# Kernel optimization log

Hardware: AMD Instinct MI355X
Metric: run time of the kernel (lower is better)

The kernel has to match this reference:

```python
import math
import jax, jax.numpy as jnp
import numpy as np

L, H, C, D, FF = 12, 12, 768, 64, 3072   # layers, heads, d_model, head_dim, 4*d_model
B, T = 2, 2048
CHUNK = 16
VP = CHUNK ** 3 + 2   # pos vocab (+BOS/EOS) = 4098
VF = 4096             # feature codebook


def setup_inputs() -> dict:
    key = jax.random.key(0)
    ks = jax.random.split(key, 16)
    s = 0.02
    return {
        "tokens": jax.random.randint(ks[0], (B, T), 0, VF, dtype=jnp.int32),
        "coords": jax.random.randint(ks[1], (B, T, 3), 0, CHUNK, dtype=jnp.int32),
        "token_type": jax.random.randint(ks[2], (B, T), 0, 2, dtype=jnp.int32),
        "pos_emb_w": jax.random.normal(ks[3], (VP, C), jnp.float32),
        "feat_emb_w": jax.random.normal(ks[4], (VF, C), jnp.float32),
        "qkv_w": jax.random.normal(ks[5], (L, 3 * C, C), jnp.float32) * s,
        "out_w": jax.random.normal(ks[6], (L, C, C), jnp.float32) * s,
        "q_scale": jnp.ones((L, D), jnp.float32),
        "k_scale": jnp.ones((L, D), jnp.float32),
        "ln1_w": jnp.ones((L, C), jnp.float32), "ln1_b": jnp.zeros((L, C), jnp.float32),
        "ln2_w": jnp.ones((L, C), jnp.float32), "ln2_b": jnp.zeros((L, C), jnp.float32),
        "fc1_w": jax.random.normal(ks[7], (L, FF, C), jnp.float32) * s,
        "fc2_w": jax.random.normal(ks[8], (L, C, FF), jnp.float32) * s,
        "res_a": jnp.ones((L,), jnp.float32), "res_m": jnp.ones((L,), jnp.float32),
        "skip_a": jnp.full((L,), 0.1, jnp.float32), "skip_m": jnp.full((L,), 0.1, jnp.float32),
        "lnf_w": jnp.ones((C,), jnp.float32), "lnf_b": jnp.zeros((C,), jnp.float32),
        "pos_head_w": jax.random.normal(ks[9], (VP, C), jnp.float32) * 0.001,
        "feat_head_w": jax.random.normal(ks[10], (VF, C), jnp.float32) * 0.001,
    }


def _ln(x, w, b):
    m = x.mean(-1, keepdims=True)
    v = ((x - m) ** 2).mean(-1, keepdims=True)
    return (x - m) / jnp.sqrt(v + 1e-5) * w + b


def _qknorm(x, scale):
    # per-head RMSNorm in fp32, eps added before sqrt (matches torch QKNorm)
    x32 = x.astype(jnp.float32)
    n = jnp.sqrt((x32 * x32).mean(-1, keepdims=True) + 1e-6)
    return x32 / n * scale


def _rope3d(x, coords):
    # x: (B,H,T,D); coords: (B,T,3) int voxel coords.
    # Split head_dim into 3 axis groups of `half` rotation pairs; tail dims pass through.
    half = D // 6            # pairs per axis (10 for D=64)
    rot = 3 * half           # total rotated pairs (30) -> 60 rotated dims, 4 untouched
    inv_freq = 1.0 / (10000.0 ** (jnp.arange(half, dtype=jnp.float32) / half))
    ang = coords.astype(jnp.float32)[..., :, None] * inv_freq      # (B,T,3,half)
    ang = ang.reshape(coords.shape[0], coords.shape[1], rot)        # (B,T,rot)
    cos = jnp.cos(ang)[:, None]                                     # (B,1,T,rot)
    sin = jnp.sin(ang)[:, None]
    xr = x[..., : 2 * rot].reshape(*x.shape[:-1], rot, 2)
    x1, x2 = xr[..., 0], xr[..., 1]
    rot_out = jnp.stack([x1 * cos - x2 * sin, x1 * sin + x2 * cos], axis=-1)
    rot_out = rot_out.reshape(*x.shape[:-1], 2 * rot)
    return jnp.concatenate([rot_out, x[..., 2 * rot:]], axis=-1)


def _forward(tokens, coords, token_type, pos_emb_w, feat_emb_w, qkv_w, out_w, q_scale,
             k_scale, ln1_w, ln1_b, ln2_w, ln2_b, fc1_w, fc2_w, res_a, res_m,
             skip_a, skip_m, lnf_w, lnf_b, pos_head_w, feat_head_w):
    is_feat = (token_type == 1)[..., None]
    x = jnp.where(is_feat,
                  feat_emb_w[jnp.clip(tokens, 0, VF - 1)],
                  pos_emb_w[jnp.clip(tokens, 0, VP - 1)])        # (B,T,C)
    mask = jnp.tril(jnp.ones((T, T), bool))
    scale = 1.0 / math.sqrt(D)

    def blk(x, p):
        qw, ow, qs, kcs, l1w, l1b, l2w, l2b, f1, f2, ra, rm, sa, sm = p
        h = _ln(x, l1w, l1b)
        qkv = h @ qw.T                                           # (B,T,3C)
        q, k, v = jnp.split(qkv, 3, axis=-1)
        to_heads = lambda t: t.reshape(B, T, H, D).transpose(0, 2, 1, 3)
        q, k, v = to_heads(q), to_heads(k), to_heads(v)
        q = _rope3d(_qknorm(q, qs), coords)
        k = _rope3d(_qknorm(k, kcs), coords)
        att = jnp.einsum('bhqd,bhkd->bhqk', q, k) * scale
        att = jax.nn.softmax(jnp.where(mask, att, -1e30), axis=-1)
        o = jnp.einsum('bhqk,bhkd->bhqd', att, v)
        o = o.transpose(0, 2, 1, 3).reshape(B, T, C) @ ow.T
        x = sa * x + ra * o
        h2 = _ln(x, l2w, l2b)
        m = jax.nn.gelu(h2 @ f1.T, approximate=False) @ f2.T
        x = sm * x + rm * m
        return x, None

    x, _ = jax.lax.scan(blk, x, (qkv_w, out_w, q_scale, k_scale, ln1_w, ln1_b,
                                 ln2_w, ln2_b, fc1_w, fc2_w, res_a, res_m,
                                 skip_a, skip_m))
    x = _ln(x, lnf_w, lnf_b)
    return x @ pos_head_w.T, x @ feat_head_w.T


def reference(tokens, coords, token_type, pos_emb_w, feat_emb_w, qkv_w, out_w,
              q_scale, k_scale, ln1_w, ln1_b, ln2_w, ln2_b, fc1_w, fc2_w,
              res_a, res_m, skip_a, skip_m, lnf_w, lnf_b, pos_head_w, feat_head_w):
    return _forward(tokens, coords, token_type, pos_emb_w, feat_emb_w, qkv_w, out_w,
                    q_scale, k_scale, ln1_w, ln1_b, ln2_w, ln2_b, fc1_w, fc2_w,
                    res_a, res_m, skip_a, skip_m, lnf_w, lnf_b, pos_head_w, feat_head_w)
```

## Files before the change

### kernel.cpp

```cpp
#include <hip/hip_runtime.h>
#include <math.h>

constexpr int B_  = 2;
constexpr int T_  = 2048;
constexpr int H_  = 12;
constexpr int C_  = 768;
constexpr int D_  = 64;
constexpr int FF_ = 3072;
constexpr int L_  = 12;
constexpr int VP_ = 4098;
constexpr int VF_ = 4096;
constexpr int BT_ = B_ * T_;

__global__ __launch_bounds__(256) void embed_kernel(
    const int* __restrict__ tokens, const int* __restrict__ ttype,
    const float* __restrict__ pos_w, const float* __restrict__ feat_w,
    float* __restrict__ x) {
  int row = blockIdx.x;
  int tok = tokens[row];
  const float* src;
  if (ttype[row] == 1) {
    int t = min(max(tok, 0), VF_ - 1);
    src = feat_w + (size_t)t * C_;
  } else {
    int t = min(max(tok, 0), VP_ - 1);
    src = pos_w + (size_t)t * C_;
  }
  float* dst = x + (size_t)row * C_;
  for (int c = threadIdx.x; c < C_; c += 256) dst[c] = src[c];
}

__global__ __launch_bounds__(256) void ln_kernel(
    const float* __restrict__ x, const float* __restrict__ w,
    const float* __restrict__ b, float* __restrict__ out) {
  int row = blockIdx.x;
  const float* xr = x + (size_t)row * C_;
  float vv[3];
  float s = 0.f, s2 = 0.f;
#pragma unroll
  for (int i = 0; i < 3; i++) {
    float t = xr[threadIdx.x + i * 256];
    vv[i] = t; s += t; s2 += t * t;
  }
#pragma unroll
  for (int off = 32; off; off >>= 1) {
    s  += __shfl_xor(s,  off, 64);
    s2 += __shfl_xor(s2, off, 64);
  }
  __shared__ float ss[4], ss2[4];
  int wave = threadIdx.x >> 6, lane = threadIdx.x & 63;
  if (lane == 0) { ss[wave] = s; ss2[wave] = s2; }
  __syncthreads();
  s  = ss[0] + ss[1] + ss[2] + ss[3];
  s2 = ss2[0] + ss2[1] + ss2[2] + ss2[3];
  float mean = s * (1.f / C_);
  float var  = s2 * (1.f / C_) - mean * mean;
  float inv  = 1.f / sqrtf(var + 1e-5f);
  float* orow = out + (size_t)row * C_;
#pragma unroll
  for (int i = 0; i < 3; i++) {
    int c = threadIdx.x + i * 256;
    orow[c] = (vv[i] - mean) * inv * w[c] + b[c];
  }
}

template <int BN, int EPI>
__global__ __launch_bounds__(256) void gemm_xwT(
    const float* __restrict__ A, const float* __restrict__ W,
    float* Co, const float* resid,
    const float* __restrict__ skip_p, const float* __restrict__ rs_p,
    int M, int N, int K) {
  constexpr int BK = 16;
  constexpr int MB = 2;
  constexpr int NB = BN / 64;
  __shared__ float As[BK][132];
  __shared__ float Ws[BK][BN + 4];

  int bm = blockIdx.y * 128, bn = blockIdx.x * BN;
  int tid = threadIdx.x;
  int tn = tid & 15, tm = tid >> 4;
  int lr = tid >> 2;
  int lk = (tid & 3) * 4;

  float acc[MB][NB][4][4] = {};
  float4 ar[MB], wr[NB];

#pragma unroll
  for (int u = 0; u < MB; u++)
    ar[u] = *(const float4*)(A + (size_t)(bm + lr + 64 * u) * K + lk);
#pragma unroll
  for (int v = 0; v < NB; v++) {
    int wrow = bn + lr + 64 * v;
    wr[v] = (wrow < N) ? *(const float4*)(W + (size_t)wrow * K + lk)
                       : make_float4(0.f, 0.f, 0.f, 0.f);
  }
#pragma unroll
  for (int u = 0; u < MB; u++) {
    As[lk + 0][lr + 64 * u] = ar[u].x; As[lk + 1][lr + 64 * u] = ar[u].y;
    As[lk + 2][lr + 64 * u] = ar[u].z; As[lk + 3][lr + 64 * u] = ar[u].w;
  }
#pragma unroll
  for (int v = 0; v < NB; v++) {
    Ws[lk + 0][lr + 64 * v] = wr[v].x; Ws[lk + 1][lr + 64 * v] = wr[v].y;
    Ws[lk + 2][lr + 64 * v] = wr[v].z; Ws[lk + 3][lr + 64 * v] = wr[v].w;
  }
  __syncthreads();

  for (int k0 = 0; k0 < K; k0 += BK) {
    bool has_next = (k0 + BK < K);
    if (has_next) {
      int kn = k0 + BK;
#pragma unroll
      for (int u = 0; u < MB; u++)
        ar[u] = *(const float4*)(A + (size_t)(bm + lr + 64 * u) * K + kn + lk);
#pragma unroll
      for (int v = 0; v < NB; v++) {
        int wrow = bn + lr + 64 * v;
        wr[v] = (wrow < N) ? *(const float4*)(W + (size_t)wrow * K + kn + lk)
                           : make_float4(0.f, 0.f, 0.f, 0.f);
      }
    }
#pragma unroll
    for (int kk = 0; kk < BK; kk++) {
      float a[MB][4], b[NB][4];
#pragma unroll
      for (int u = 0; u < MB; u++) {
        float4 a4 = *(const float4*)&As[kk][u * 64 + tm * 4];
        a[u][0] = a4.x; a[u][1] = a4.y; a[u][2] = a4.z; a[u][3] = a4.w;
      }
#pragma unroll
      for (int v = 0; v < NB; v++) {
        float4 b4 = *(const float4*)&Ws[kk][v * 64 + tn * 4];
        b[v][0] = b4.x; b[v][1] = b4.y; b[v][2] = b4.z; b[v][3] = b4.w;
      }
#pragma unroll
      for (int u = 0; u < MB; u++)
#pragma unroll
        for (int v = 0; v < NB; v++)
#pragma unroll
          for (int i = 0; i < 4; i++)
#pragma unroll
            for (int j = 0; j < 4; j++)
              acc[u][v][i][j] += a[u][i] * b[v][j];
    }
    if (has_next) {
      __syncthreads();
#pragma unroll
      for (int u = 0; u < MB; u++) {
        As[lk + 0][lr + 64 * u] = ar[u].x; As[lk + 1][lr + 64 * u] = ar[u].y;
        As[lk + 2][lr + 64 * u] = ar[u].z; As[lk + 3][lr + 64 * u] = ar[u].w;
      }
#pragma unroll
      for (int v = 0; v < NB; v++) {
        Ws[lk + 0][lr + 64 * v] = wr[v].x; Ws[lk + 1][lr + 64 * v] = wr[v].y;
        Ws[lk + 2][lr + 64 * v] = wr[v].z; Ws[lk + 3][lr + 64 * v] = wr[v].w;
      }
      __syncthreads();
    }
  }

  float skip = 0.f, rs = 0.f;
  if constexpr (EPI == 2) { skip = *skip_p; rs = *rs_p; }
  bool full = (bn + BN <= N) && ((N & 3) == 0);
#pragma unroll
  for (int u = 0; u < MB; u++)
#pragma unroll
    for (int i = 0; i < 4; i++) {
      int m = bm + u * 64 + tm * 4 + i;
#pragma unroll
      for (int v = 0; v < NB; v++) {
        int n = bn + v * 64 + tn * 4;
        float c4[4];
#pragma unroll
        for (int j = 0; j < 4; j++) {
          float c = acc[u][v][i][j];
          if constexpr (EPI == 1)
            c = 0.5f * c * (1.f + erff(c * 0.70710678118654752f));
          if constexpr (EPI == 2) {
            if (n + j < N) c = skip * resid[(size_t)m * N + n + j] + rs * c;
          }
          c4[j] = c;
        }
        if (full) {
          *(float4*)(Co + (size_t)m * N + n) =
              make_float4(c4[0], c4[1], c4[2], c4[3]);
        } else {
#pragma unroll
          for (int j = 0; j < 4; j++)
            if (n + j < N) Co[(size_t)m * N + n + j] = c4[j];
        }
      }
    }
}

__global__ __launch_bounds__(256) void qknorm_rope_kernel(
    float* __restrict__ qkv, const int* __restrict__ coords,
    const float* __restrict__ qscale, const float* __restrict__ kscale) {
  int row = blockIdx.x;
  int wave = threadIdx.x >> 6, lane = threadIdx.x & 63;
  int c0 = coords[row * 3 + 0];
  int c1 = coords[row * 3 + 1];
  int c2 = coords[row * 3 + 2];
  for (int g = wave; g < 2 * H_; g += 4) {
    int h = g >> 1, isk = g & 1;
    size_t idx = (size_t)row * (3 * C_) + (size_t)isk * C_ + h * D_ + lane;
    float v = qkv[idx];
    float ssum = v * v;
#pragma unroll
    for (int off = 32; off; off >>= 1) ssum += __shfl_xor(ssum, off, 64);
    float n = sqrtf(ssum * (1.f / D_) + 1e-6f);
    const float* sc = isk ? kscale : qscale;
    float xn = v / n * sc[lane];
    float partner = __shfl_xor(xn, 1, 64);
    float outv = xn;
    if (lane < 60) {
      int p = lane >> 1;
      int axis = p / 10;
      int f = p - axis * 10;
      int crd = (axis == 0) ? c0 : ((axis == 1) ? c1 : c2);
      float invf = expf(-(float)f * 0.1f * 9.210340371976184f);
      float ang = (float)crd * invf;
      float sn, cs;
      sincosf(ang, &sn, &cs);
      if (lane & 1) {
        outv = partner * sn + xn * cs;
      } else {
        outv = xn * cs - partner * sn;
      }
    }
    qkv[idx] = outv;
  }
}

__global__ __launch_bounds__(256) void attn_kernel(
    const float* __restrict__ qkv, float* __restrict__ out) {
  int bh = blockIdx.y;
  int b = bh / H_, h = bh % H_;
  int q0 = blockIdx.x * 64;
  int tid = threadIdx.x;
  int tn = tid & 15, tm = tid >> 4;

  __shared__ float Qs[64][72];
  __shared__ float Ks[64][72];
  __shared__ float Vs[64][72];
  __shared__ float Ps[64][72];

  {
    int lr = tid >> 2;
    int ld = (tid & 3) * 16;
    const float* src = qkv + (size_t)(b * T_ + q0 + lr) * (3 * C_) + h * D_ + ld;
    const float sc = 0.125f;
#pragma unroll
    for (int u = 0; u < 4; u++) {
      float4 v = ((const float4*)src)[u];
      Qs[ld + u * 4 + 0][lr] = v.x * sc;
      Qs[ld + u * 4 + 1][lr] = v.y * sc;
      Qs[ld + u * 4 + 2][lr] = v.z * sc;
      Qs[ld + u * 4 + 3][lr] = v.w * sc;
    }
  }

  float accO[4][4] = {};
  float mrow[4], lrow[4];
#pragma unroll
  for (int i = 0; i < 4; i++) { mrow[i] = -1e30f; lrow[i] = 0.f; }

  for (int k0 = 0; k0 <= q0; k0 += 64) {
    __syncthreads();
    {
      int lr = tid >> 2;
      int ld = (tid & 3) * 16;
      const float* kb = qkv + (size_t)(b * T_ + k0 + lr) * (3 * C_) + C_ + h * D_ + ld;
#pragma unroll
      for (int u = 0; u < 4; u++) {
        float4 v = ((const float4*)kb)[u];
        Ks[ld + u * 4 + 0][lr] = v.x;
        Ks[ld + u * 4 + 1][lr] = v.y;
        Ks[ld + u * 4 + 2][lr] = v.z;
        Ks[ld + u * 4 + 3][lr] = v.w;
      }
      const float* vb = kb + C_;
#pragma unroll
      for (int u = 0; u < 4; u++) {
        *(float4*)&Vs[lr][ld + u * 4] = ((const float4*)vb)[u];
      }
    }
    __syncthreads();

    float s[4][4] = {};
#pragma unroll
    for (int d = 0; d < 64; d++) {
      float4 a4 = *(const float4*)&Qs[d][tm * 4];
      float4 b4 = *(const float4*)&Ks[d][tn * 4];
      float a[4] = {a4.x, a4.y, a4.z, a4.w};
      float bb[4] = {b4.x, b4.y, b4.z, b4.w};
#pragma unroll
      for (int i = 0; i < 4; i++)
#pragma unroll
        for (int j = 0; j < 4; j++) s[i][j] += a[i] * bb[j];
    }

    if (k0 == q0) {
#pragma unroll
      for (int i = 0; i < 4; i++)
#pragma unroll
        for (int j = 0; j < 4; j++)
          if (tn * 4 + j > tm * 4 + i) s[i][j] = -1e30f;
    }

#pragma unroll
    for (int i = 0; i < 4; i++) {
      float rm = fmaxf(fmaxf(s[i][0], s[i][1]), fmaxf(s[i][2], s[i][3]));
#pragma unroll
      for (int off = 1; off < 16; off <<= 1) rm = fmaxf(rm, __shfl_xor(rm, off, 64));
      float mnew = fmaxf(mrow[i], rm);
      float alpha = __expf(mrow[i] - mnew);
      mrow[i] = mnew;
      float rs = 0.f;
#pragma unroll
      for (int j = 0; j < 4; j++) {
        float p = __expf(s[i][j] - mnew);
        s[i][j] = p;
        rs += p;
      }
#pragma unroll
      for (int off = 1; off < 16; off <<= 1) rs += __shfl_xor(rs, off, 64);
      lrow[i] = lrow[i] * alpha + rs;
#pragma unroll
      for (int j = 0; j < 4; j++) accO[i][j] *= alpha;
    }

#pragma unroll
    for (int i = 0; i < 4; i++)
      *(float4*)&Ps[tm * 4 + i][tn * 4] = make_float4(s[i][0], s[i][1], s[i][2], s[i][3]);
    __syncthreads();

#pragma unroll
    for (int kk = 0; kk < 64; kk += 4) {
      float pi[4][4], vu[4][4];
#pragma unroll
      for (int i = 0; i < 4; i++) {
        float4 p4 = *(const float4*)&Ps[tm * 4 + i][kk];
        pi[i][0] = p4.x; pi[i][1] = p4.y; pi[i][2] = p4.z; pi[i][3] = p4.w;
      }
#pragma unroll
      for (int u = 0; u < 4; u++) {
        float4 v4 = *(const float4*)&Vs[kk + u][tn * 4];
        vu[u][0] = v4.x; vu[u][1] = v4.y; vu[u][2] = v4.z; vu[u][3] = v4.w;
      }
#pragma unroll
      for (int u = 0; u < 4; u++)
#pragma unroll
        for (int i = 0; i < 4; i++)
#pragma unroll
          for (int j = 0; j < 4; j++) accO[i][j] += pi[i][u] * vu[u][j];
    }
  }

#pragma unroll
  for (int i = 0; i < 4; i++) {
    float inv = 1.f / lrow[i];
    float4 o = make_float4(accO[i][0] * inv, accO[i][1] * inv,
                           accO[i][2] * inv, accO[i][3] * inv);
    *(float4*)(out + (size_t)(b * T_ + q0 + tm * 4 + i) * C_ + h * D_ + tn * 4) = o;
  }
}

extern "C" void kernel_launch(void* const* d_in, const int* in_sizes, int n_in,
                              void* d_out, int out_size, void* d_ws, size_t ws_size,
                              hipStream_t stream) {
  const int*   tokens    = (const int*)d_in[0];
  const int*   coords    = (const int*)d_in[1];
  const int*   ttype     = (const int*)d_in[2];
  const float* pos_emb   = (const float*)d_in[3];
  const float* feat_emb  = (const float*)d_in[4];
  const float* qkv_w     = (const float*)d_in[5];
  const float* out_w     = (const float*)d_in[6];
  const float* q_scale   = (const float*)d_in[7];
  const float* k_scale   = (const float*)d_in[8];
  const float* ln1_w     = (const float*)d_in[9];
  const float* ln1_b     = (const float*)d_in[10];
  const float* ln2_w     = (const float*)d_in[11];
  const float* ln2_b     = (const float*)d_in[12];
  const float* fc1_w     = (const float*)d_in[13];
  const float* fc2_w     = (const float*)d_in[14];
  const float* res_a     = (const float*)d_in[15];
  const float* res_m     = (const float*)d_in[16];
  const float* skip_a    = (const float*)d_in[17];
  const float* skip_m    = (const float*)d_in[18];
  const float* lnf_w     = (const float*)d_in[19];
  const float* lnf_b     = (const float*)d_in[20];
  const float* pos_head  = (const float*)d_in[21];
  const float* feat_head = (const float*)d_in[22];
  float* out = (float*)d_out;

  float* ws    = (float*)d_ws;
  float* x     = ws;
  float* hbuf  = x     + (size_t)BT_ * C_;
  float* qkvb  = hbuf  + (size_t)BT_ * C_;
  float* attnb = qkvb  + (size_t)BT_ * 3 * C_;
  float* ffb   = attnb + (size_t)BT_ * C_;

  embed_kernel<<<BT_, 256, 0, stream>>>(tokens, ttype, pos_emb, feat_emb, x);

  for (int l = 0; l < L_; l++) {
    ln_kernel<<<BT_, 256, 0, stream>>>(x, ln1_w + l * C_, ln1_b + l * C_, hbuf);
    gemm_xwT<128, 0><<<dim3((3 * C_) / 128, BT_ / 128), 256, 0, stream>>>(
        hbuf, qkv_w + (size_t)l * 3 * C_ * C_, qkvb, nullptr, nullptr, nullptr,
        BT_, 3 * C_, C_);
    qknorm_rope_kernel<<<BT_, 256, 0, stream>>>(qkvb, coords,
                                                q_scale + l * D_, k_scale + l * D_);
    attn_kernel<<<dim3(T_ / 64, B_ * H_), 256, 0, stream>>>(qkvb, attnb);
    gemm_xwT<64, 2><<<dim3(C_ / 64, BT_ / 128), 256, 0, stream>>>(
        attnb, out_w + (size_t)l * C_ * C_, x, x, skip_a + l, res_a + l,
        BT_, C_, C_);
    ln_kernel<<<BT_, 256, 0, stream>>>(x, ln2_w + l * C_, ln2_b + l * C_, hbuf);
    gemm_xwT<128, 1><<<dim3(FF_ / 128, BT_ / 128), 256, 0, stream>>>(
        hbuf, fc1_w + (size_t)l * FF_ * C_, ffb, nullptr, nullptr, nullptr,
        BT_, FF_, C_);
    gemm_xwT<64, 2><<<dim3(C_ / 64, BT_ / 128), 256, 0, stream>>>(
        ffb, fc2_w + (size_t)l * C_ * FF_, x, x, skip_m + l, res_m + l,
        BT_, C_, FF_);
  }

  ln_kernel<<<BT_, 256, 0, stream>>>(x, lnf_w, lnf_b, hbuf);
  gemm_xwT<128, 0><<<dim3((VP_ + 127) / 128, BT_ / 128), 256, 0, stream>>>(
      hbuf, pos_head, out, nullptr, nullptr, nullptr, BT_, VP_, C_);
  gemm_xwT<128, 0><<<dim3(VF_ / 128, BT_ / 128), 256, 0, stream>>>(
      hbuf, feat_head, out + (size_t)BT_ * VP_, nullptr, nullptr, nullptr,
      BT_, VF_, C_);
}
```

Before: 16.04 ms.

## Register-prefetch next K/V tile in attention and swizzle shared-memory layouts

```diff
diff --git a/kernel.cpp b/kernel.cpp
--- a/kernel.cpp
+++ b/kernel.cpp
@@ -232,6 +232,8 @@
   }
 }
 
+constexpr int SK_ = 76;
+
 __global__ __launch_bounds__(256) void attn_kernel(
     const float* __restrict__ qkv, float* __restrict__ out) {
   int bh = blockIdx.y;
@@ -239,26 +241,48 @@
   int q0 = blockIdx.x * 64;
   int tid = threadIdx.x;
   int tn = tid & 15, tm = tid >> 4;
-
-  __shared__ float Qs[64][72];
-  __shared__ float Ks[64][72];
-  __shared__ float Vs[64][72];
-  __shared__ float Ps[64][72];
+  int lr = tid >> 2;
+  int q4 = (tid & 3) * 4;
+
+  __shared__ float Qs[64 * SK_];
+  __shared__ float Ks[64 * SK_];
+  __shared__ float Vs[64 * SK_];
+  __shared__ float Ps[64 * SK_];
 
   {
-    int lr = tid >> 2;
-    int ld = (tid & 3) * 16;
-    const float* src = qkv + (size_t)(b * T_ + q0 + lr) * (3 * C_) + h * D_ + ld;
+    const float* qsrc = qkv + (size_t)(b * T_ + q0 + lr) * (3 * C_) + h * D_ + q4;
     const float sc = 0.125f;
 #pragma unroll
     for (int u = 0; u < 4; u++) {
-      float4 v = ((const float4*)src)[u];
-      Qs[ld + u * 4 + 0][lr] = v.x * sc;
-      Qs[ld + u * 4 + 1][lr] = v.y * sc;
-      Qs[ld + u * 4 + 2][lr] = v.z * sc;
-      Qs[ld + u * 4 + 3][lr] = v.w * sc;
-    }
-  }
+      float4 v = *(const float4*)(qsrc + u * 16);
+      int d = q4 + u * 16;
+      Qs[(d + 0) * SK_ + lr] = v.x * sc;
+      Qs[(d + 1) * SK_ + lr] = v.y * sc;
+      Qs[(d + 2) * SK_ + lr] = v.z * sc;
+      Qs[(d + 3) * SK_ + lr] = v.w * sc;
+    }
+  }
+  float4 kreg[4], vreg[4];
+  {
+    const float* kb = qkv + (size_t)(b * T_ + lr) * (3 * C_) + C_ + h * D_ + q4;
+#pragma unroll
+    for (int u = 0; u < 4; u++) kreg[u] = *(const float4*)(kb + u * 16);
+    const float* vb = kb + C_;
+#pragma unroll
+    for (int u = 0; u < 4; u++) vreg[u] = *(const float4*)(vb + u * 16);
+  }
+#pragma unroll
+  for (int u = 0; u < 4; u++) {
+    int d = q4 + u * 16;
+    Ks[(d + 0) * SK_ + lr] = kreg[u].x;
+    Ks[(d + 1) * SK_ + lr] = kreg[u].y;
+    Ks[(d + 2) * SK_ + lr] = kreg[u].z;
+    Ks[(d + 3) * SK_ + lr] = kreg[u].w;
+  }
+#pragma unroll
+  for (int u = 0; u < 4; u++)
+    *(float4*)&Vs[lr * SK_ + ((q4 + u * 16) ^ ((lr & 7) << 2))] = vreg[u];
+  __syncthreads();
 
   float accO[4][4] = {};
   float mrow[4], lrow[4];
@@ -266,32 +290,22 @@
   for (int i = 0; i < 4; i++) { mrow[i] = -1e30f; lrow[i] = 0.f; }
 
   for (int k0 = 0; k0 <= q0; k0 += 64) {
-    __syncthreads();
-    {
-      int lr = tid >> 2;
-      int ld = (tid & 3) * 16;
-      const float* kb = qkv + (size_t)(b * T_ + k0 + lr) * (3 * C_) + C_ + h * D_ + ld;
-#pragma unroll
-      for (int u = 0; u < 4; u++) {
-        float4 v = ((const float4*)kb)[u];
-        Ks[ld + u * 4 + 0][lr] = v.x;
-        Ks[ld + u * 4 + 1][lr] = v.y;
-        Ks[ld + u * 4 + 2][lr] = v.z;
-        Ks[ld + u * 4 + 3][lr] = v.w;
-      }
+    bool more = (k0 + 64 <= q0);
+    if (more) {
+      const float* kb =
+          qkv + (size_t)(b * T_ + k0 + 64 + lr) * (3 * C_) + C_ + h * D_ + q4;
+#pragma unroll
+      for (int u = 0; u < 4; u++) kreg[u] = *(const float4*)(kb + u * 16);
       const float* vb = kb + C_;
 #pragma unroll
-      for (int u = 0; u < 4; u++) {
-        *(float4*)&Vs[lr][ld + u * 4] = ((const float4*)vb)[u];
-      }
-    }
-    __syncthreads();
+      for (int u = 0; u < 4; u++) vreg[u] = *(const float4*)(vb + u * 16);
+    }
 
     float s[4][4] = {};
 #pragma unroll
     for (int d = 0; d < 64; d++) {
-      float4 a4 = *(const float4*)&Qs[d][tm * 4];
-      float4 b4 = *(const float4*)&Ks[d][tn * 4];
+      float4 a4 = *(const float4*)&Qs[d * SK_ + tm * 4];
+      float4 b4 = *(const float4*)&Ks[d * SK_ + tn * 4];
       float a[4] = {a4.x, a4.y, a4.z, a4.w};
       float bb[4] = {b4.x, b4.y, b4.z, b4.w};
 #pragma unroll
@@ -331,21 +345,37 @@
     }
 
 #pragma unroll
-    for (int i = 0; i < 4; i++)
-      *(float4*)&Ps[tm * 4 + i][tn * 4] = make_float4(s[i][0], s[i][1], s[i][2], s[i][3]);
+    for (int i = 0; i < 4; i++) {
+      int r = tm * 4 + i;
+      *(float4*)&Ps[r * SK_ + ((tn * 4) ^ ((r & 7) << 2))] =
+          make_float4(s[i][0], s[i][1], s[i][2], s[i][3]);
+    }
     __syncthreads();
+
+    if (more) {
+#pragma unroll
+      for (int u = 0; u < 4; u++) {
+        int d = q4 + u * 16;
+        Ks[(d + 0) * SK_ + lr] = kreg[u].x;
+        Ks[(d + 1) * SK_ + lr] = kreg[u].y;
+        Ks[(d + 2) * SK_ + lr] = kreg[u].z;
+        Ks[(d + 3) * SK_ + lr] = kreg[u].w;
+      }
+    }
 
 #pragma unroll
     for (int kk = 0; kk < 64; kk += 4) {
       float pi[4][4], vu[4][4];
 #pragma unroll
       for (int i = 0; i < 4; i++) {
-        float4 p4 = *(const float4*)&Ps[tm * 4 + i][kk];
+        int r = tm * 4 + i;
+        float4 p4 = *(const float4*)&Ps[r * SK_ + (kk ^ ((r & 7) << 2))];
         pi[i][0] = p4.x; pi[i][1] = p4.y; pi[i][2] = p4.z; pi[i][3] = p4.w;
       }
 #pragma unroll
       for (int u = 0; u < 4; u++) {
-        float4 v4 = *(const float4*)&Vs[kk + u][tn * 4];
+        int k = kk + u;
+        float4 v4 = *(const float4*)&Vs[k * SK_ + ((tn * 4) ^ ((k & 7) << 2))];
         vu[u][0] = v4.x; vu[u][1] = v4.y; vu[u][2] = v4.z; vu[u][3] = v4.w;
       }
 #pragma unroll
@@ -354,6 +384,13 @@
         for (int i = 0; i < 4; i++)
 #pragma unroll
           for (int j = 0; j < 4; j++) accO[i][j] += pi[i][u] * vu[u][j];
+    }
+    __syncthreads();
+
+    if (more) {
+#pragma unroll
+      for (int u = 0; u < 4; u++)
+        *(float4*)&Vs[lr * SK_ + ((q4 + u * 16) ^ ((lr & 7) << 2))] = vreg[u];
     }
   }
 
```

New measurement: 16.20 ms. No clear change (+1.0%).

## Replace FP32 SIMT GEMMs with split-bf16 MFMA GEMM (3-pass hi/lo)

Applied to the files above, without the earlier changes.

```diff
diff --git a/kernel.cpp b/kernel.cpp
--- a/kernel.cpp
+++ b/kernel.cpp
@@ -11,6 +11,9 @@
 constexpr int VP_ = 4098;
 constexpr int VF_ = 4096;
 constexpr int BT_ = B_ * T_;
+
+typedef __attribute__((ext_vector_type(8))) short bf16x8;
+typedef __attribute__((ext_vector_type(4))) float f32x4;
 
 __global__ __launch_bounds__(256) void embed_kernel(
     const int* __restrict__ tokens, const int* __restrict__ ttype,
@@ -64,96 +67,122 @@
   }
 }
 
-template <int BN, int EPI>
-__global__ __launch_bounds__(256) void gemm_xwT(
+__device__ inline void cvt4(float4 v, unsigned int hi[2], unsigned int lo[2]) {
+  unsigned int b0 = __float_as_uint(v.x), b1 = __float_as_uint(v.y);
+  unsigned int b2 = __float_as_uint(v.z), b3 = __float_as_uint(v.w);
+  hi[0] = (b0 >> 16) | (b1 & 0xFFFF0000u);
+  hi[1] = (b2 >> 16) | (b3 & 0xFFFF0000u);
+  float h0 = __uint_as_float(b0 & 0xFFFF0000u);
+  float h1 = __uint_as_float(b1 & 0xFFFF0000u);
+  float h2 = __uint_as_float(b2 & 0xFFFF0000u);
+  float h3 = __uint_as_float(b3 & 0xFFFF0000u);
+  unsigned int l0 = __float_as_uint(v.x - h0);
+  unsigned int l1 = __float_as_uint(v.y - h1);
+  unsigned int l2 = __float_as_uint(v.z - h2);
+  unsigned int l3 = __float_as_uint(v.w - h3);
+  lo[0] = (l0 >> 16) | (l1 & 0xFFFF0000u);
+  lo[1] = (l2 >> 16) | (l3 & 0xFFFF0000u);
+}
+
+template <int EPI>
+__global__ __launch_bounds__(256) void gemm_mfma(
     const float* __restrict__ A, const float* __restrict__ W,
     float* Co, const float* resid,
     const float* __restrict__ skip_p, const float* __restrict__ rs_p,
     int M, int N, int K) {
-  constexpr int BK = 16;
-  constexpr int MB = 2;
-  constexpr int NB = BN / 64;
-  __shared__ float As[BK][132];
-  __shared__ float Ws[BK][BN + 4];
-
-  int bm = blockIdx.y * 128, bn = blockIdx.x * BN;
+  constexpr int SR = 40;
+  __shared__ unsigned short AsH[128 * SR];
+  __shared__ unsigned short AsL[128 * SR];
+  __shared__ unsigned short WsH[128 * SR];
+  __shared__ unsigned short WsL[128 * SR];
+
+  int bm = blockIdx.y * 128, bn = blockIdx.x * 128;
   int tid = threadIdx.x;
-  int tn = tid & 15, tm = tid >> 4;
-  int lr = tid >> 2;
-  int lk = (tid & 3) * 4;
-
-  float acc[MB][NB][4][4] = {};
-  float4 ar[MB], wr[NB];
-
-#pragma unroll
-  for (int u = 0; u < MB; u++)
-    ar[u] = *(const float4*)(A + (size_t)(bm + lr + 64 * u) * K + lk);
-#pragma unroll
-  for (int v = 0; v < NB; v++) {
-    int wrow = bn + lr + 64 * v;
-    wr[v] = (wrow < N) ? *(const float4*)(W + (size_t)wrow * K + lk)
-                       : make_float4(0.f, 0.f, 0.f, 0.f);
-  }
-#pragma unroll
-  for (int u = 0; u < MB; u++) {
-    As[lk + 0][lr + 64 * u] = ar[u].x; As[lk + 1][lr + 64 * u] = ar[u].y;
-    As[lk + 2][lr + 64 * u] = ar[u].z; As[lk + 3][lr + 64 * u] = ar[u].w;
-  }
-#pragma unroll
-  for (int v = 0; v < NB; v++) {
-    Ws[lk + 0][lr + 64 * v] = wr[v].x; Ws[lk + 1][lr + 64 * v] = wr[v].y;
-    Ws[lk + 2][lr + 64 * v] = wr[v].z; Ws[lk + 3][lr + 64 * v] = wr[v].w;
+  int lane = tid & 63, wv = tid >> 6;
+  int wm = (wv >> 1) * 64, wn = (wv & 1) * 64;
+  int fr = lane & 15;
+  int ko = (lane >> 4) * 8;
+
+  int srow = tid >> 1;
+  int skq  = (tid & 1) * 4;
+
+  f32x4 acc[4][4] = {};
+  float4 apf[4], wpf[4];
+
+  const float* Arow = A + (size_t)(bm + srow) * K + skq * 4;
+  const float* Wrow = W + (size_t)(bn + srow) * K + skq * 4;
+  bool wvalid = (bn + srow) < N;
+
+#pragma unroll
+  for (int u = 0; u < 4; u++) {
+    apf[u] = *(const float4*)(Arow + u * 4);
+    wpf[u] = wvalid ? *(const float4*)(Wrow + u * 4)
+                    : make_float4(0.f, 0.f, 0.f, 0.f);
+  }
+  {
+    unsigned int h[2], l[2];
+#pragma unroll
+    for (int u = 0; u < 4; u++) {
+      int off = srow * SR + (skq + u) * 4;
+      cvt4(apf[u], h, l);
+      *(uint2*)&AsH[off] = make_uint2(h[0], h[1]);
+      *(uint2*)&AsL[off] = make_uint2(l[0], l[1]);
+      cvt4(wpf[u], h, l);
+      *(uint2*)&WsH[off] = make_uint2(h[0], h[1]);
+      *(uint2*)&WsL[off] = make_uint2(l[0], l[1]);
+    }
   }
   __syncthreads();
 
-  for (int k0 = 0; k0 < K; k0 += BK) {
-    bool has_next = (k0 + BK < K);
+  const unsigned short* aHp = &AsH[(wm + fr) * SR + ko];
+  const unsigned short* aLp = &AsL[(wm + fr) * SR + ko];
+  const unsigned short* bHp = &WsH[(wn + fr) * SR + ko];
+  const unsigned short* bLp = &WsL[(wn + fr) * SR + ko];
+
+  for (int k0 = 0; k0 < K; k0 += 32) {
+    bool has_next = (k0 + 32 < K);
     if (has_next) {
-      int kn = k0 + BK;
-#pragma unroll
-      for (int u = 0; u < MB; u++)
-        ar[u] = *(const float4*)(A + (size_t)(bm + lr + 64 * u) * K + kn + lk);
-#pragma unroll
-      for (int v = 0; v < NB; v++) {
-        int wrow = bn + lr + 64 * v;
-        wr[v] = (wrow < N) ? *(const float4*)(W + (size_t)wrow * K + kn + lk)
-                           : make_float4(0.f, 0.f, 0.f, 0.f);
-      }
-    }
-#pragma unroll
-    for (int kk = 0; kk < BK; kk++) {
-      float a[MB][4], b[NB][4];
-#pragma unroll
-      for (int u = 0; u < MB; u++) {
-        float4 a4 = *(const float4*)&As[kk][u * 64 + tm * 4];
-        a[u][0] = a4.x; a[u][1] = a4.y; a[u][2] = a4.z; a[u][3] = a4.w;
-      }
-#pragma unroll
-      for (int v = 0; v < NB; v++) {
-        float4 b4 = *(const float4*)&Ws[kk][v * 64 + tn * 4];
-        b[v][0] = b4.x; b[v][1] = b4.y; b[v][2] = b4.z; b[v][3] = b4.w;
-      }
-#pragma unroll
-      for (int u = 0; u < MB; u++)
-#pragma unroll
-        for (int v = 0; v < NB; v++)
-#pragma unroll
-          for (int i = 0; i < 4; i++)
-#pragma unroll
-            for (int j = 0; j < 4; j++)
-              acc[u][v][i][j] += a[u][i] * b[v][j];
-    }
+#pragma unroll
+      for (int u = 0; u < 4; u++) {
+        apf[u] = *(const float4*)(Arow + k0 + 32 + u * 4);
+        wpf[u] = wvalid ? *(const float4*)(Wrow + k0 + 32 + u * 4)
+                        : make_float4(0.f, 0.f, 0.f, 0.f);
+      }
+    }
+
+    bf16x8 aH[4], aL[4];
+#pragma unroll
+    for (int fm = 0; fm < 4; fm++) {
+      aH[fm] = *(const bf16x8*)(aHp + fm * 16 * SR);
+      aL[fm] = *(const bf16x8*)(aLp + fm * 16 * SR);
+    }
+#pragma unroll
+    for (int fn = 0; fn < 4; fn++) {
+      bf16x8 bH = *(const bf16x8*)(bHp + fn * 16 * SR);
+      bf16x8 bL = *(const bf16x8*)(bLp + fn * 16 * SR);
+#pragma unroll
+      for (int fm = 0; fm < 4; fm++) {
+        acc[fm][fn] = __builtin_amdgcn_mfma_f32_16x16x32_bf16(
+            aH[fm], bH, acc[fm][fn], 0, 0, 0);
+        acc[fm][fn] = __builtin_amdgcn_mfma_f32_16x16x32_bf16(
+            aH[fm], bL, acc[fm][fn], 0, 0, 0);
+        acc[fm][fn] = __builtin_amdgcn_mfma_f32_16x16x32_bf16(
+            aL[fm], bH, acc[fm][fn], 0, 0, 0);
+      }
+    }
+
     if (has_next) {
       __syncthreads();
-#pragma unroll
-      for (int u = 0; u < MB; u++) {
-        As[lk + 0][lr + 64 * u] = ar[u].x; As[lk + 1][lr + 64 * u] = ar[u].y;
-        As[lk + 2][lr + 64 * u] = ar[u].z; As[lk + 3][lr + 64 * u] = ar[u].w;
-      }
-#pragma unroll
-      for (int v = 0; v < NB; v++) {
-        Ws[lk + 0][lr + 64 * v] = wr[v].x; Ws[lk + 1][lr + 64 * v] = wr[v].y;
-        Ws[lk + 2][lr + 64 * v] = wr[v].z; Ws[lk + 3][lr + 64 * v] = wr[v].w;
+      unsigned int h[2], l[2];
+#pragma unroll
+      for (int u = 0; u < 4; u++) {
+        int off = srow * SR + (skq + u) * 4;
+        cvt4(apf[u], h, l);
+        *(uint2*)&AsH[off] = make_uint2(h[0], h[1]);
+        *(uint2*)&AsL[off] = make_uint2(l[0], l[1]);
+        cvt4(wpf[u], h, l);
+        *(uint2*)&WsH[off] = make_uint2(h[0], h[1]);
+        *(uint2*)&WsL[off] = make_uint2(l[0], l[1]);
       }
       __syncthreads();
     }
@@ -161,36 +190,25 @@
 
   float skip = 0.f, rs = 0.f;
   if constexpr (EPI == 2) { skip = *skip_p; rs = *rs_p; }
-  bool full = (bn + BN <= N) && ((N & 3) == 0);
-#pragma unroll
-  for (int u = 0; u < MB; u++)
-#pragma unroll
-    for (int i = 0; i < 4; i++) {
-      int m = bm + u * 64 + tm * 4 + i;
-#pragma unroll
-      for (int v = 0; v < NB; v++) {
-        int n = bn + v * 64 + tn * 4;
-        float c4[4];
-#pragma unroll
-        for (int j = 0; j < 4; j++) {
-          float c = acc[u][v][i][j];
-          if constexpr (EPI == 1)
-            c = 0.5f * c * (1.f + erff(c * 0.70710678118654752f));
-          if constexpr (EPI == 2) {
-            if (n + j < N) c = skip * resid[(size_t)m * N + n + j] + rs * c;
-          }
-          c4[j] = c;
-        }
-        if (full) {
-          *(float4*)(Co + (size_t)m * N + n) =
-              make_float4(c4[0], c4[1], c4[2], c4[3]);
-        } else {
-#pragma unroll
-          for (int j = 0; j < 4; j++)
-            if (n + j < N) Co[(size_t)m * N + n + j] = c4[j];
-        }
-      }
-    }
+#pragma unroll
+  for (int fn = 0; fn < 4; fn++) {
+    int col = bn + wn + fn * 16 + fr;
+    if (col >= N) continue;
+#pragma unroll
+    for (int fm = 0; fm < 4; fm++) {
+      f32x4 c = acc[fm][fn];
+#pragma unroll
+      for (int j = 0; j < 4; j++) {
+        int row = bm + wm + fm * 16 + (lane >> 4) * 4 + j;
+        float cv = c[j];
+        if constexpr (EPI == 1)
+          cv = 0.5f * cv * (1.f + erff(cv * 0.70710678118654752f));
+        if constexpr (EPI == 2)
+          cv = skip * resid[(size_t)row * N + col] + rs * cv;
+        Co[(size_t)row * N + col] = cv;
+      }
+    }
+  }
 }
 
 __global__ __launch_bounds__(256) void qknorm_rope_kernel(
@@ -405,28 +423,28 @@
 
   for (int l = 0; l < L_; l++) {
     ln_kernel<<<BT_, 256, 0, stream>>>(x, ln1_w + l * C_, ln1_b + l * C_, hbuf);
-    gemm_xwT<128, 0><<<dim3((3 * C_) / 128, BT_ / 128), 256, 0, stream>>>(
+    gemm_mfma<0><<<dim3((3 * C_) / 128, BT_ / 128), 256, 0, stream>>>(
         hbuf, qkv_w + (size_t)l * 3 * C_ * C_, qkvb, nullptr, nullptr, nullptr,
         BT_, 3 * C_, C_);
     qknorm_rope_kernel<<<BT_, 256, 0, stream>>>(qkvb, coords,
                                                 q_scale + l * D_, k_scale + l * D_);
     attn_kernel<<<dim3(T_ / 64, B_ * H_), 256, 0, stream>>>(qkvb, attnb);
-    gemm_xwT<64, 2><<<dim3(C_ / 64, BT_ / 128), 256, 0, stream>>>(
+    gemm_mfma<2><<<dim3(C_ / 128, BT_ / 128), 256, 0, stream>>>(
         attnb, out_w + (size_t)l * C_ * C_, x, x, skip_a + l, res_a + l,
         BT_, C_, C_);
     ln_kernel<<<BT_, 256, 0, stream>>>(x, ln2_w + l * C_, ln2_b + l * C_, hbuf);
-    gemm_xwT<128, 1><<<dim3(FF_ / 128, BT_ / 128), 256, 0, stream>>>(
+    gemm_mfma<1><<<dim3(FF_ / 128, BT_ / 128), 256, 0, stream>>>(
         hbuf, fc1_w + (size_t)l * FF_ * C_, ffb, nullptr, nullptr, nullptr,
         BT_, FF_, C_);
-    gemm_xwT<64, 2><<<dim3(C_ / 64, BT_ / 128), 256, 0, stream>>>(
+    gemm_mfma<2><<<dim3(C_ / 128, BT_ / 128), 256, 0, stream>>>(
         ffb, fc2_w + (size_t)l * C_ * FF_, x, x, skip_m + l, res_m + l,
         BT_, C_, FF_);
   }
 
   ln_kernel<<<BT_, 256, 0, stream>>>(x, lnf_w, lnf_b, hbuf);
-  gemm_xwT<128, 0><<<dim3((VP_ + 127) / 128, BT_ / 128), 256, 0, stream>>>(
+  gemm_mfma<0><<<dim3((VP_ + 127) / 128, BT_ / 128), 256, 0, stream>>>(
       hbuf, pos_head, out, nullptr, nullptr, nullptr, BT_, VP_, C_);
-  gemm_xwT<128, 0><<<dim3(VF_ / 128, BT_ / 128), 256, 0, stream>>>(
+  gemm_mfma<0><<<dim3(VF_ / 128, BT_ / 128), 256, 0, stream>>>(
       hbuf, feat_head, out + (size_t)BT_ * VP_, nullptr, nullptr, nullptr,
       BT_, VF_, C_);
 }
```

Result: faster. 13.01 ms (-18.9%).
